# Kernel optimization log

Hardware: AMD Instinct MI355X
Metric: run time of the kernel (lower is better)

Reference implementation:

```python
import jax, jax.numpy as jnp
import numpy as np

BINS = 64


def _histogram(x, bins=BINS):
    """Faithful jax version of ColorHistogramLoss.get_histogram.

    Original semantics: edges = linspace(-1, 1, bins); bin j (j < bins-1) counts
    edges[j] <= v < edges[j+1]; last bin counts v >= edges[-1] (= 1).
    Values v < -1 fall in no bin. Single bucketize + scatter-add pass.
    """
    B, C = x.shape[0], x.shape[1]
    xf = x.reshape(B * C, -1)            # [B*C, N]
    N = xf.shape[1]
    edges = jnp.linspace(-1.0, 1.0, bins).astype(x.dtype)
    # searchsorted(side='right') - 1 gives j with edges[j] <= v < edges[j+1];
    # v < -1 -> -1 (invalid); v >= 1 -> bins-1 after clip (matches open last bin).
    idx = jnp.searchsorted(edges, xf, side='right') - 1
    valid = idx >= 0
    idx = jnp.clip(idx, 0, bins - 1)
    seg = idx + jnp.arange(B * C)[:, None] * bins      # per-(batch,channel) offset
    counts = jax.ops.segment_sum(
        valid.astype(jnp.float32).ravel(), seg.ravel(),
        num_segments=B * C * bins)
    return counts.reshape(B, C * bins) / N             # [B, C*bins]


def setup_inputs() -> dict:
    key = jax.random.key(0)
    k1, k2 = jax.random.split(key)
    shape = (32, 3, 512, 512)
    # pixels normalized to [-1, 1), matching the linspace(-1, 1) bin edges
    inp = jax.random.uniform(k1, shape, dtype=jnp.float32) * 2.0 - 1.0
    tgt = jax.random.uniform(k2, shape, dtype=jnp.float32) * 2.0 - 1.0
    return {"input": inp, "target": tgt}


def reference(input, target):
    hist_in = _histogram(input, BINS)
    hist_tgt = _histogram(target, BINS)
    return jnp.mean(jnp.abs(hist_in - hist_tgt))   # F.l1_loss (mean reduction)
```

## Files before the change

kernel.cpp:

```cpp
#include <hip/hip_runtime.h>


#define BINS 64
#define PLANES 96
#define PLANE_F4 65536
#define SEGS 32
#define SEG_F4 2048
#define TPB 256
#define F4T 8

__device__ __forceinline__ void bump(int* lh, float v, int inc) {
    int bin = (int)floorf((v + 1.0f) * 31.5f);
    if (bin >= 0) {
        bin = bin > 63 ? 63 : bin;
        atomicAdd(&lh[bin], inc);
    }
}

__global__ __launch_bounds__(TPB) void hist_diff_kernel(
        const float4* __restrict__ in4, const float4* __restrict__ tg4,
        int* __restrict__ gdiff) {
    __shared__ int lh[BINS];
    const int tid = threadIdx.x;
    if (tid < BINS) lh[tid] = 0;
    __syncthreads();

    const int plane = blockIdx.x >> 5;
    const int seg   = blockIdx.x & (SEGS - 1);
    const long base = (long)plane * PLANE_F4 + (long)seg * SEG_F4 + tid;

    float4 a[F4T];
#pragma unroll
    for (int k = 0; k < F4T; ++k) a[k] = in4[base + k * TPB];
#pragma unroll
    for (int k = 0; k < F4T; ++k) {
        bump(lh, a[k].x, 1); bump(lh, a[k].y, 1);
        bump(lh, a[k].z, 1); bump(lh, a[k].w, 1);
    }
#pragma unroll
    for (int k = 0; k < F4T; ++k) a[k] = tg4[base + k * TPB];
#pragma unroll
    for (int k = 0; k < F4T; ++k) {
        bump(lh, a[k].x, -1); bump(lh, a[k].y, -1);
        bump(lh, a[k].z, -1); bump(lh, a[k].w, -1);
    }

    __syncthreads();
    if (tid < BINS) {
        int v = lh[tid];
        if (v != 0) atomicAdd(&gdiff[plane * BINS + tid], v);
    }
}

__global__ __launch_bounds__(TPB) void reduce_abs_kernel(
        const int* __restrict__ gdiff, float* __restrict__ out) {
    int s = 0;
    for (int i = threadIdx.x; i < PLANES * BINS; i += TPB) {
        int v = gdiff[i];
        s += (v < 0) ? -v : v;
    }
#pragma unroll
    for (int off = 32; off > 0; off >>= 1) s += __shfl_down(s, off, 64);
    __shared__ int ws[TPB / 64];
    const int wid  = threadIdx.x >> 6;
    const int lane = threadIdx.x & 63;
    if (lane == 0) ws[wid] = s;
    __syncthreads();
    if (threadIdx.x == 0) {
        int total = 0;
#pragma unroll
        for (int w = 0; w < TPB / 64; ++w) total += ws[w];
        out[0] = (float)total * (1.0f / (262144.0f * 6144.0f));
    }
}

extern "C" void kernel_launch(void* const* d_in, const int* in_sizes, int n_in,
                              void* d_out, int out_size, void* d_ws, size_t ws_size,
                              hipStream_t stream) {
    const float4* inp = (const float4*)d_in[0];
    const float4* tgt = (const float4*)d_in[1];
    int* gdiff = (int*)d_ws;

    hipMemsetAsync(gdiff, 0, PLANES * BINS * sizeof(int), stream);
    hist_diff_kernel<<<PLANES * SEGS, TPB, 0, stream>>>(inp, tgt, gdiff);
    reduce_abs_kernel<<<1, TPB, 0, stream>>>(gdiff, (float*)d_out);
}
```

Before: 214.4 us.

## Replace shared-memory atomic histogram with wave ballot bin matching

```diff
diff --git a/kernel.cpp b/kernel.cpp
--- a/kernel.cpp
+++ b/kernel.cpp
@@ -9,47 +9,53 @@
 #define TPB 256
 #define F4T 8
 
-__device__ __forceinline__ void bump(int* lh, float v, int inc) {
-    int bin = (int)floorf((v + 1.0f) * 31.5f);
-    if (bin >= 0) {
-        bin = bin > 63 ? 63 : bin;
-        atomicAdd(&lh[bin], inc);
-    }
-}
-
 __global__ __launch_bounds__(TPB) void hist_diff_kernel(
         const float4* __restrict__ in4, const float4* __restrict__ tg4,
         int* __restrict__ gdiff) {
-    __shared__ int lh[BINS];
-    const int tid = threadIdx.x;
-    if (tid < BINS) lh[tid] = 0;
-    __syncthreads();
-
+    const int tid  = threadIdx.x;
+    const int lane = tid & 63;
     const int plane = blockIdx.x >> 5;
     const int seg   = blockIdx.x & (SEGS - 1);
     const long base = (long)plane * PLANE_F4 + (long)seg * SEG_F4 + tid;
 
-    float4 a[F4T];
+    unsigned long long inv[6];
+#pragma unroll
+    for (int k = 0; k < 6; ++k)
+        inv[k] = ((lane >> k) & 1) ? 0ull : ~0ull;
+
+    float4 a[F4T], b[F4T];
 #pragma unroll
     for (int k = 0; k < F4T; ++k) a[k] = in4[base + k * TPB];
 #pragma unroll
+    for (int k = 0; k < F4T; ++k) b[k] = tg4[base + k * TPB];
+
+    int cin = 0, ctg = 0;
+    auto slot = [&](float v, int& cnt) {
+        float x = (v + 1.0f) * 31.5f;
+        int bin = (int)x;
+        bin = bin > 63 ? 63 : bin;
+        unsigned long long m =
+            (__ballot(bin & 1)  ^ inv[0]) &
+            (__ballot(bin & 2)  ^ inv[1]) &
+            (__ballot(bin & 4)  ^ inv[2]) &
+            (__ballot(bin & 8)  ^ inv[3]) &
+            (__ballot(bin & 16) ^ inv[4]) &
+            (__ballot(bin & 32) ^ inv[5]);
+        cnt += __popcll(m);
+    };
+#pragma unroll
     for (int k = 0; k < F4T; ++k) {
-        bump(lh, a[k].x, 1); bump(lh, a[k].y, 1);
-        bump(lh, a[k].z, 1); bump(lh, a[k].w, 1);
+        slot(a[k].x, cin); slot(a[k].y, cin);
+        slot(a[k].z, cin); slot(a[k].w, cin);
     }
 #pragma unroll
-    for (int k = 0; k < F4T; ++k) a[k] = tg4[base + k * TPB];
-#pragma unroll
     for (int k = 0; k < F4T; ++k) {
-        bump(lh, a[k].x, -1); bump(lh, a[k].y, -1);
-        bump(lh, a[k].z, -1); bump(lh, a[k].w, -1);
+        slot(b[k].x, ctg); slot(b[k].y, ctg);
+        slot(b[k].z, ctg); slot(b[k].w, ctg);
     }
 
-    __syncthreads();
-    if (tid < BINS) {
-        int v = lh[tid];
-        if (v != 0) atomicAdd(&gdiff[plane * BINS + tid], v);
-    }
+    const int d = cin - ctg;
+    if (d != 0) atomicAdd(&gdiff[plane * BINS + lane], d);
 }
 
 __global__ __launch_bounds__(TPB) void reduce_abs_kernel(
```

After: 226.2 us. +5.5%, slower.
